# Optimization experiments

Hardware: AMD Instinct MI355X
Metric: run time of the kernel (lower is better)

## Reference

```python
import jax, jax.numpy as jnp
import numpy as np

EMBED_DIM = 1024
NUM_HEADS = 16
N_POS = 2048
BATCH = 4


def setup_inputs() -> dict:
    key = jax.random.key(0)
    k_x, k_w1, k_b1, k_wo, k_bo = jax.random.split(key, 5)
    s1 = 1.0 / np.sqrt(EMBED_DIM)
    x = jax.random.normal(k_x, (BATCH, N_POS, EMBED_DIM), dtype=jnp.float32)
    # torch Linear weights stored as [in, out] for x @ W + b
    W_qkv = jax.random.uniform(k_w1, (EMBED_DIM, 3 * EMBED_DIM), dtype=jnp.float32, minval=-s1, maxval=s1)
    b_qkv = jax.random.uniform(k_b1, (3 * EMBED_DIM,), dtype=jnp.float32, minval=-s1, maxval=s1)
    W_o = jax.random.uniform(k_wo, (EMBED_DIM, EMBED_DIM), dtype=jnp.float32, minval=-s1, maxval=s1)
    b_o = jax.random.uniform(k_bo, (EMBED_DIM,), dtype=jnp.float32, minval=-s1, maxval=s1)
    return {"x": x, "W_qkv": W_qkv, "b_qkv": b_qkv, "W_o": W_o, "b_o": b_o}


def reference(x, W_qkv, b_qkv, W_o, b_o):
    B, N, C = x.shape
    H = NUM_HEADS
    d_k = C // H
    qkv = x @ W_qkv + b_qkv                       # [B, N, 3C]
    q, k, v = jnp.split(qkv, 3, axis=-1)
    q = q.reshape(B, N, H, d_k).transpose(0, 2, 1, 3)  # [B, H, N, d_k]
    k = k.reshape(B, N, H, d_k).transpose(0, 2, 1, 3)
    v = v.reshape(B, N, H, d_k).transpose(0, 2, 1, 3)
    scores = jnp.einsum('bhqd,bhkd->bhqk', q, k) * (1.0 / np.sqrt(d_k))
    causal = jnp.tril(jnp.ones((N, N), dtype=bool))
    scores = jnp.where(causal, scores, -jnp.inf)
    attn = jax.nn.softmax(scores, axis=-1)
    out = jnp.einsum('bhqk,bhkd->bhqd', attn, v)  # [B, H, N, d_k]
    out = out.transpose(0, 2, 1, 3).reshape(B, N, C)
    return out @ W_o + b_o
```

## Files before the change

kernel.cpp:

```cpp
#include <hip/hip_runtime.h>
#include <hip/hip_bf16.h>

typedef __attribute__((ext_vector_type(8))) __bf16 bf16x8;
typedef __attribute__((ext_vector_type(4))) float f32x4;
typedef __attribute__((ext_vector_type(16))) float f32x16;
typedef __attribute__((ext_vector_type(4))) unsigned short u16x4;
typedef __attribute__((ext_vector_type(8))) unsigned short u16x8;
typedef __attribute__((ext_vector_type(4))) unsigned int u32x4;
typedef unsigned short u16;

#define MFMA16 __builtin_amdgcn_mfma_f32_16x16x32_bf16
#define MFMA32 __builtin_amdgcn_mfma_f32_32x32x16_bf16

#if __has_builtin(__builtin_amdgcn_exp2f)
#define EXP2F __builtin_amdgcn_exp2f
#else
#define EXP2F(x) __expf((x) * 0.69314718056f)
#endif

__device__ inline u16 f32_to_bf16_bits(float f) {
    unsigned u = __builtin_bit_cast(unsigned, f);
    unsigned r = u + 0x7FFFu + ((u >> 16) & 1u);
    return (u16)(r >> 16);
}

__device__ inline void g2l16(const void* g, void* l) {
    __builtin_amdgcn_global_load_lds(
        (const __attribute__((address_space(1))) unsigned int*)g,
        (__attribute__((address_space(3))) unsigned int*)l,
        16, 0, 0);
}

__device__ inline float red32_max(float x) { return fmaxf(x, __shfl_xor(x, 32)); }
__device__ inline float red32_sum(float x) { return x + __shfl_xor(x, 32); }

__global__ void cvt_bf16_kernel(const float* __restrict__ in, u16* __restrict__ out, int n) {
    int i = (blockIdx.x * 256 + threadIdx.x) * 8;
    if (i >= n) return;
    f32x4 v0 = *(const f32x4*)&in[i];
    f32x4 v1 = *(const f32x4*)&in[i + 4];
    u16x8 r;
#pragma unroll
    for (int j = 0; j < 4; ++j) {
        r[j] = f32_to_bf16_bits(v0[j]);
        r[j + 4] = f32_to_bf16_bits(v1[j]);
    }
    *(u16x8*)&out[i] = r;
}

__global__ __launch_bounds__(256) void cvt_t2_kernel(
    const float* __restrict__ W1, u16* __restrict__ WT1, int N1,
    const float* __restrict__ W2, u16* __restrict__ WT2, int N2, int K)
{
    int bx = blockIdx.x;
    const float* W; u16* WT; int N;
    const int nb1 = N1 >> 6;
    if (bx < nb1) { W = W1; WT = WT1; N = N1; }
    else          { W = W2; WT = WT2; N = N2; bx -= nb1; }
    const int w = threadIdx.x >> 6, l = threadIdx.x & 63;
    const int n = bx * 64 + l;
    const int k0 = blockIdx.y * 32 + w * 8;
    u16x8 r;
#pragma unroll
    for (int i = 0; i < 8; ++i)
        r[i] = f32_to_bf16_bits(W[(size_t)(k0 + i) * N + n]);
    *(u16x8*)&WT[(size_t)n * K + k0] = r;
}

template <int STORE_BF16>
__global__ __launch_bounds__(512) void gemm_8p2(
    const u16* __restrict__ A, const u16* __restrict__ BT,
    const float* __restrict__ bias, void* __restrict__ Cv,
    int M, int N, int K, int qcols, float qscale)
{
    __shared__ __align__(16) u16 SM[49152];
    const int tid = threadIdx.x;
    const int w = tid >> 6, l = tid & 63;
    const int lr = l & 15, lh = l >> 4;
    const int wr = (w >> 2) * 64;
    const int wc = (w & 3) * 64;

    const int xcd = blockIdx.x & 7;
    const int jb = blockIdx.x >> 3;
    const int g = jb >> 4;
    const int r = jb & 15;
    const int m0 = (xcd * 8 + (r >> 1)) * 128;
    const int n0 = (g * 2 + (r & 1)) * 256;

    const int NT = K >> 6;

    const int f0 = tid, f1 = 512 + tid;
    const int r0 = f0 >> 3, r1 = f1 >> 3;
    const int c0 = ((f0 & 7) ^ (r0 & 7)) * 8;

#define STAGE_CHUNK(j, c)                                                       \
    do {                                                                        \
        const int kk_ = (j) * 64;                                               \
        u16* db_ = SM + (((j) & 1) * 24576) + (c) * 8192;                       \
        const u16* base_ = ((c) == 0) ? (A + (size_t)m0 * K)                    \
                                      : (BT + (size_t)(n0 + ((c)-1) * 128) * K);\
        g2l16(base_ + (size_t)r0 * K + kk_ + c0, db_ + f0 * 8);                 \
        g2l16(base_ + (size_t)r1 * K + kk_ + c0, db_ + f1 * 8);                 \
    } while (0)

    f32x4 acc[4][4];
#pragma unroll
    for (int m = 0; m < 4; ++m)
#pragma unroll
        for (int n = 0; n < 4; ++n) acc[m][n] = (f32x4)(0.0f);

    STAGE_CHUNK(0, 0); STAGE_CHUNK(0, 1); STAGE_CHUNK(0, 2);

    const int swk = lr & 7;
    for (int j = 0; j < NT; ++j) {
        const u16* Ab = SM + (j & 1) * 24576;
        const u16* Bb = Ab + 8192;

        if (j + 1 < NT) {
            STAGE_CHUNK(j + 1, 0);
            asm volatile("s_waitcnt vmcnt(2)\n\ts_barrier" ::: "memory");
        } else {
            asm volatile("s_waitcnt vmcnt(0)\n\ts_barrier" ::: "memory");
        }

        bf16x8 af[4][2], bfr[2][2];
#pragma unroll
        for (int m = 0; m < 4; ++m) {
            const int row = wr + m * 16 + lr;
#pragma unroll
            for (int ks = 0; ks < 2; ++ks)
                af[m][ks] = *(const bf16x8*)&Ab[row * 64 + (((ks * 4 + lh) ^ swk) << 3)];
        }
#pragma unroll
        for (int n = 0; n < 2; ++n) {
            const int row = wc + n * 16 + lr;
#pragma unroll
            for (int ks = 0; ks < 2; ++ks)
                bfr[n][ks] = *(const bf16x8*)&Bb[row * 64 + (((ks * 4 + lh) ^ swk) << 3)];
        }
        if (j + 1 < NT) STAGE_CHUNK(j + 1, 1);

        asm volatile("s_barrier\n\ts_waitcnt lgkmcnt(0)" ::: "memory");
        __builtin_amdgcn_s_setprio(1);
#pragma unroll
        for (int m = 0; m < 4; ++m)
#pragma unroll
            for (int n = 0; n < 2; ++n)
#pragma unroll
                for (int ks = 0; ks < 2; ++ks)
                    acc[m][n] = MFMA16(af[m][ks], bfr[n][ks], acc[m][n], 0, 0, 0);
        __builtin_amdgcn_s_setprio(0);
        asm volatile("s_barrier" ::: "memory");

#pragma unroll
        for (int n = 0; n < 2; ++n) {
            const int row = wc + (n + 2) * 16 + lr;
#pragma unroll
            for (int ks = 0; ks < 2; ++ks)
                bfr[n][ks] = *(const bf16x8*)&Bb[row * 64 + (((ks * 4 + lh) ^ swk) << 3)];
        }
        if (j + 1 < NT) STAGE_CHUNK(j + 1, 2);

        asm volatile("s_barrier\n\ts_waitcnt lgkmcnt(0)" ::: "memory");
        __builtin_amdgcn_s_setprio(1);
#pragma unroll
        for (int m = 0; m < 4; ++m)
#pragma unroll
            for (int n = 0; n < 2; ++n)
#pragma unroll
                for (int ks = 0; ks < 2; ++ks)
                    acc[m][n + 2] = MFMA16(af[m][ks], bfr[n][ks], acc[m][n + 2], 0, 0, 0);
        __builtin_amdgcn_s_setprio(0);
        asm volatile("s_barrier" ::: "memory");
    }
#undef STAGE_CHUNK

#pragma unroll
    for (int m = 0; m < 4; ++m) {
        int row = m0 + wr + m * 16 + lh * 4;
#pragma unroll
        for (int n = 0; n < 4; ++n) {
            int col = n0 + wc + n * 16 + lr;
            float bs = bias[col];
            float sc = (col < qcols) ? qscale : 1.0f;
#pragma unroll
            for (int j2 = 0; j2 < 4; ++j2) {
                float v = (acc[m][n][j2] + bs) * sc;
                if (STORE_BF16)
                    ((u16*)Cv)[(size_t)(row + j2) * N + col] = f32_to_bf16_bits(v);
                else
                    ((float*)Cv)[(size_t)(row + j2) * N + col] = v;
            }
        }
    }
}

template <int STORE_BF16>
__global__ __launch_bounds__(256) void gemm_nt(
    const u16* __restrict__ A, const u16* __restrict__ BT,
    const float* __restrict__ bias, void* __restrict__ Cv,
    int M, int N, int K, int qcols, float qscale, int nbx)
{
    __shared__ __align__(16) u16 SM[24576];
    const int tid = threadIdx.x;
    const int w = tid >> 6, l = tid & 63;
    const int lr = l & 15, lh = l >> 4;
    const int wr = (w >> 1) * 64, wc = (w & 1) * 64;

    const int xcd = blockIdx.x & 7;
    const int j = blockIdx.x >> 3;
    const int g = j >> 5;
    const int r = j & 31;
    const int m0 = (xcd * 8 + (r >> 2)) * 128;
    const int n0 = (g * 4 + (r & 3)) * 128;
    (void)nbx;

    const int NT = K >> 5;

    const int f0 = tid, f1 = 256 + tid;
    const int r0 = f0 >> 2, r1 = f1 >> 2;
    const int cs0 = ((f0 & 3) ^ ((r0 >> 1) & 3)) * 8;
    const int cs1 = ((f1 & 3) ^ ((r1 >> 1) & 3)) * 8;
    const size_t arow0 = (size_t)(m0 + r0) * K, arow1 = (size_t)(m0 + r1) * K;
    const size_t brow0 = (size_t)(n0 + r0) * K, brow1 = (size_t)(n0 + r1) * K;

#define STAGE_TILE(t, set)                                                     \
    do {                                                                       \
        const int kk_ = (t) * 32;                                              \
        u16* dst_ = SM + (set) * 8192 + w * 512;                               \
        g2l16(A + arow0 + kk_ + cs0, dst_);                                    \
        g2l16(BT + brow0 + kk_ + cs0, dst_ + 4096);                            \
        g2l16(A + arow1 + kk_ + cs1, dst_ + 2048);                             \
        g2l16(BT + brow1 + kk_ + cs1, dst_ + 4096 + 2048);                     \
    } while (0)

    f32x4 acc[4][4];
#pragma unroll
    for (int m = 0; m < 4; ++m)
#pragma unroll
        for (int n = 0; n < 4; ++n) acc[m][n] = (f32x4)(0.0f);

    STAGE_TILE(0, 0);
    STAGE_TILE(1, 1);
    asm volatile("s_waitcnt vmcnt(4) lgkmcnt(0)\n\ts_barrier" ::: "memory");

    const int csw = (lr >> 1) & 3;
    int s0 = 0, s2 = 2;
    for (int t = 0; t < NT; ++t) {
        if (t + 2 < NT) STAGE_TILE(t + 2, s2);

        const u16* As = SM + s0 * 8192;
        const u16* Bs = As + 4096;
        bf16x8 af[4], bfr[4];
#pragma unroll
        for (int m = 0; m < 4; ++m)
            af[m] = *(const bf16x8*)&As[(wr + m * 16 + lr) * 32 + ((lh ^ csw) << 3)];
#pragma unroll
        for (int n = 0; n < 4; ++n)
            bfr[n] = *(const bf16x8*)&Bs[(wc + n * 16 + lr) * 32 + ((lh ^ csw) << 3)];
        __builtin_amdgcn_s_setprio(1);
#pragma unroll
        for (int m = 0; m < 4; ++m)
#pragma unroll
            for (int n = 0; n < 4; ++n)
                acc[m][n] = MFMA16(af[m], bfr[n], acc[m][n], 0, 0, 0);
        __builtin_amdgcn_s_setprio(0);

        if (t + 2 < NT)
            asm volatile("s_waitcnt vmcnt(4) lgkmcnt(0)\n\ts_barrier" ::: "memory");
        else if (t + 1 < NT)
            asm volatile("s_waitcnt vmcnt(0) lgkmcnt(0)\n\ts_barrier" ::: "memory");

        s0 = (s0 == 2) ? 0 : s0 + 1;
        s2 = (s2 == 2) ? 0 : s2 + 1;
    }
#undef STAGE_TILE

#pragma unroll
    for (int m = 0; m < 4; ++m) {
        int row = m0 + wr + m * 16 + lh * 4;
#pragma unroll
        for (int n = 0; n < 4; ++n) {
            int col = n0 + wc + n * 16 + lr;
            float bs = bias[col];
            float sc = (col < qcols) ? qscale : 1.0f;
#pragma unroll
            for (int j2 = 0; j2 < 4; ++j2) {
                float v = (acc[m][n][j2] + bs) * sc;
                if (STORE_BF16)
                    ((u16*)Cv)[(size_t)(row + j2) * N + col] = f32_to_bf16_bits(v);
                else
                    ((float*)Cv)[(size_t)(row + j2) * N + col] = v;
            }
        }
    }
}

__global__ __launch_bounds__(512, 1) void attn_kernel(
    const u16* __restrict__ qkv, u16* __restrict__ ctx)
{
    __shared__ __align__(16) u16 SM[32768];

    const int bid = blockIdx.x;
    const int xcd = bid & 7, jj = bid >> 3;
    const int bh = xcd * 8 + (jj >> 2);
    const int pr = jj & 3;
    const int b = bh >> 4, h = bh & 15;
    const size_t rowbase = (size_t)b * 2048;
    const int tid = threadIdx.x, w = tid >> 6, l = tid & 63;
    const int lq = l & 31, lk = l >> 5;

    const int rsub = l >> 3;
    const int cstage = l & 7;
    const int kchunk = cstage ^ rsub;

    bf16x8 vreg[2];

#pragma unroll
    for (int pass = 0; pass < 2; ++pass) {
        const int qt = pass ? (7 - pr) : pr;
        const int q0 = qt * 256;
        const int nt = 2 * qt + 2;
        const int qbase = q0 + w * 32;

        const u16* qp = qkv + (rowbase + qbase + lq) * 3072 + h * 64 + lk * 8;
        bf16x8 qf[4];
#pragma unroll
        for (int j = 0; j < 4; ++j) qf[j] = *(const bf16x8*)(qp + j * 16);

        f32x16 ot[2];
#pragma unroll
        for (int dt = 0; dt < 2; ++dt) ot[dt] = (f32x16)(0.0f);
        float m_run = -3e38f, l_run = 0.0f;

        __syncthreads();
#pragma unroll
        for (int p = 0; p < 2; ++p) {
            const int r = w * 16 + p * 8 + rsub;
            g2l16(qkv + (rowbase + r) * 3072 + 1024 + h * 64 + kchunk * 8,
                  SM + w * 1024 + p * 512);
            vreg[p] = *(const bf16x8*)(qkv + (rowbase + r) * 3072 + 2048 + h * 64 + cstage * 8);
        }
        asm volatile("s_waitcnt vmcnt(0)" ::: "memory");
#pragma unroll
        for (int p = 0; p < 2; ++p) {
            const int r = w * 16 + p * 8 + rsub;
#pragma unroll
            for (int i = 0; i < 8; ++i) {
                const int d = cstage * 8 + i;
                SM[16384 + ((d * 128 + r) ^ (((i ^ cstage) & 7) << 3))] = ((const u16*)&vreg[p])[i];
            }
        }
        __syncthreads();

        for (int t = 0; t < nt; ++t) {
            const int c = t & 1;
            const int kb = t * 128;
            u16* const Kb = SM + (c ? 8192 : 0);
            u16* const Vb = SM + 16384 + (c ? 8192 : 0);

            if (t + 1 < nt) {
                const int kb2 = kb + 128;
#pragma unroll
                for (int p = 0; p < 2; ++p) {
                    const int r = w * 16 + p * 8 + rsub;
                    g2l16(qkv + (rowbase + kb2 + r) * 3072 + 1024 + h * 64 + kchunk * 8,
                          SM + (c ? 0 : 8192) + w * 1024 + p * 512);
                    vreg[p] = *(const bf16x8*)(qkv + (rowbase + kb2 + r) * 3072 + 2048 + h * 64 + cstage * 8);
                }
            }

            if (kb <= qbase + 31) {
                bf16x8 kf[4][4];
#pragma unroll
                for (int kt = 0; kt < 4; ++kt)
#pragma unroll
                    for (int j = 0; j < 4; ++j)
                        kf[kt][j] = *(const bf16x8*)&Kb[((kt * 32 + lq) * 64 + j * 16 + lk * 8) ^ ((lq & 7) << 3)];

                f32x16 sf[4];
                __builtin_amdgcn_s_setprio(1);
#pragma unroll
                for (int kt = 0; kt < 4; ++kt) {
                    f32x16 z = (f32x16)(0.0f);
#pragma unroll
                    for (int j = 0; j < 4; ++j) z = MFMA32(kf[kt][j], qf[j], z, 0, 0, 0);
                    sf[kt] = z;
                }
                __builtin_amdgcn_s_setprio(0);

                float mt = -3e38f;
                if (kb + 127 > qbase) {
                    const int qrow = qbase + lq;
#pragma unroll
                    for (int kt = 0; kt < 4; ++kt)
#pragma unroll
                        for (int r = 0; r < 16; ++r) {
                            const int key = kb + kt * 32 + (r & 3) + 8 * (r >> 2) + 4 * lk;
                            float v = sf[kt][r];
                            if (key > qrow) v = -3e38f;
                            sf[kt][r] = v;
                            mt = fmaxf(mt, v);
                        }
                } else {
#pragma unroll
                    for (int kt = 0; kt < 4; ++kt)
#pragma unroll
                        for (int r = 0; r < 16; ++r) mt = fmaxf(mt, sf[kt][r]);
                }
                mt = red32_max(mt);

                const bool defer = __all(mt <= m_run + 16.0f);
                float mn = m_run;
                if (!defer) {
                    mn = fmaxf(m_run, mt);
                    const float alpha = EXP2F(m_run - mn);
                    m_run = mn;
                    l_run *= alpha;
#pragma unroll
                    for (int dt = 0; dt < 2; ++dt)
#pragma unroll
                        for (int r = 0; r < 16; ++r) ot[dt][r] *= alpha;
                }
                float rs = 0.0f;
#pragma unroll
                for (int kt = 0; kt < 4; ++kt)
#pragma unroll
                    for (int r = 0; r < 16; ++r) {
                        const float pp = EXP2F(sf[kt][r] - mn);
                        sf[kt][r] = pp;
                        rs += pp;
                    }
                l_run += red32_sum(rs);

                unsigned pc[4][4][2];
#pragma unroll
                for (int kt = 0; kt < 4; ++kt)
#pragma unroll
                    for (int rg = 0; rg < 4; ++rg) {
                        unsigned d0, d1;
                        asm("v_cvt_pk_bf16_f32 %0, %1, %2"
                            : "=v"(d0) : "v"((float)sf[kt][rg * 4 + 0]), "v"((float)sf[kt][rg * 4 + 1]));
                        asm("v_cvt_pk_bf16_f32 %0, %1, %2"
                            : "=v"(d1) : "v"((float)sf[kt][rg * 4 + 2]), "v"((float)sf[kt][rg * 4 + 3]));
                        pc[kt][rg][0] = d0;
                        pc[kt][rg][1] = d1;
                    }

                __builtin_amdgcn_s_setprio(1);
#pragma unroll
                for (int kt = 0; kt < 4; ++kt)
#pragma unroll
                    for (int hh = 0; hh < 2; ++hh) {
                        unsigned a0 = pc[kt][2 * hh][0], a1 = pc[kt][2 * hh][1];
                        unsigned b0 = pc[kt][2 * hh + 1][0], b1 = pc[kt][2 * hh + 1][1];
                        asm("v_permlane32_swap_b32 %0, %1" : "+v"(a0), "+v"(b0));
                        asm("v_permlane32_swap_b32 %0, %1" : "+v"(a1), "+v"(b1));
                        u32x4 wv = {a0, a1, b0, b1};
                        const bf16x8 pb = __builtin_bit_cast(bf16x8, wv);
                        const int k0 = 2 * kt + hh;
#pragma unroll
                        for (int dt = 0; dt < 2; ++dt) {
                            const int d = dt * 32 + lq;
                            const int vswz = ((d & 7) ^ (d >> 3)) & 7;
                            const bf16x8 vf = *(const bf16x8*)&Vb[((d * 128) + (k0 * 16 + lk * 8)) ^ (vswz << 3)];
                            ot[dt] = MFMA32(vf, pb, ot[dt], 0, 0, 0);
                        }
                    }
                __builtin_amdgcn_s_setprio(0);
            }

            asm volatile("s_waitcnt vmcnt(0)" ::: "memory");
            if (t + 1 < nt) {
                u16* const Vn = SM + 16384 + (c ? 0 : 8192);
#pragma unroll
                for (int p = 0; p < 2; ++p) {
                    const int r = w * 16 + p * 8 + rsub;
#pragma unroll
                    for (int i = 0; i < 8; ++i) {
                        const int d = cstage * 8 + i;
                        Vn[((d * 128 + r) ^ (((i ^ cstage) & 7) << 3))] = ((const u16*)&vreg[p])[i];
                    }
                }
            }
            __syncthreads();
        }

        u16* const out_l = SM + w * 2176;
        const float inv = 1.0f / l_run;
#pragma unroll
        for (int dt = 0; dt < 2; ++dt)
#pragma unroll
            for (int r = 0; r < 16; ++r) {
                const int d = dt * 32 + (r & 3) + 8 * (r >> 2) + 4 * lk;
                out_l[lq * 68 + d] = f32_to_bf16_bits(ot[dt][r] * inv);
            }
#pragma unroll
        for (int rr = 0; rr < 4; ++rr) {
            const int row = rr * 8 + (l >> 3);
            const bf16x8 v = *(const bf16x8*)&out_l[row * 68 + (l & 7) * 8];
            *(bf16x8*)(ctx + (rowbase + qbase + row) * 1024 + h * 64 + (l & 7) * 8) = v;
        }
    }
}

extern "C" void kernel_launch(void* const* d_in, const int* in_sizes, int n_in,
                              void* d_out, int out_size, void* d_ws, size_t ws_size,
                              hipStream_t stream) {
    const float* x      = (const float*)d_in[0];
    const float* W_qkv  = (const float*)d_in[1];
    const float* b_qkv  = (const float*)d_in[2];
    const float* W_o    = (const float*)d_in[3];
    const float* b_o    = (const float*)d_in[4];
    float* out = (float*)d_out;

    const int M = 4 * 2048;
    const int C = 1024;
    u16* qkv   = (u16*)d_ws;
    u16* xb    = qkv   + (size_t)M * 3 * C;
    u16* wqkvt = xb    + (size_t)M * C;
    u16* ctx   = wqkvt + (size_t)3 * C * C;
    u16* wot   = ctx   + (size_t)M * C;

    const float SCQ = 0.125f * 1.44269504089f;

    cvt_bf16_kernel<<<(M * C) / (256 * 8), 256, 0, stream>>>(x, xb, M * C);
    cvt_t2_kernel<<<dim3(3 * C / 64 + C / 64, C / 32), 256, 0, stream>>>(
        W_qkv, wqkvt, 3 * C, W_o, wot, C, C);

    gemm_8p2<1><<<(M / 128) * (3 * C / 256), 512, 0, stream>>>(xb, wqkvt, b_qkv, qkv,
                                                               M, 3 * C, C, C, SCQ);

    attn_kernel<<<256, 512, 0, stream>>>(qkv, ctx);

    gemm_nt<0><<<(C / 128) * (M / 128), 256, 0, stream>>>(ctx, wot, b_o, out,
                                                          M, C, C, 0, 1.0f, C / 128);
}
```

Measured before the change: 160.7 us.

## Split attention passes into separate blocks and reuse 8-phase GEMM for output projection

The attention kernel no longer loops over two causal query tiles per block. It launches 512 blocks, each handling one tile, with launch bounds allowing two blocks per CU, which aims for more occupancy and better overlap between blocks. The output projection now uses the existing gemm_8p2 kernel with 256-wide tiles instead of the separate gemm_nt kernel, and gemm_nt is removed. The risk is register pressure under the 2-block bound, and losing the paired light/heavy tile balance inside each block.

```diff
diff --git a/kernel.cpp b/kernel.cpp
--- a/kernel.cpp
+++ b/kernel.cpp
@@ -195,116 +195,18 @@
     }
 }
 
-template <int STORE_BF16>
-__global__ __launch_bounds__(256) void gemm_nt(
-    const u16* __restrict__ A, const u16* __restrict__ BT,
-    const float* __restrict__ bias, void* __restrict__ Cv,
-    int M, int N, int K, int qcols, float qscale, int nbx)
-{
-    __shared__ __align__(16) u16 SM[24576];
-    const int tid = threadIdx.x;
-    const int w = tid >> 6, l = tid & 63;
-    const int lr = l & 15, lh = l >> 4;
-    const int wr = (w >> 1) * 64, wc = (w & 1) * 64;
-
-    const int xcd = blockIdx.x & 7;
-    const int j = blockIdx.x >> 3;
-    const int g = j >> 5;
-    const int r = j & 31;
-    const int m0 = (xcd * 8 + (r >> 2)) * 128;
-    const int n0 = (g * 4 + (r & 3)) * 128;
-    (void)nbx;
-
-    const int NT = K >> 5;
-
-    const int f0 = tid, f1 = 256 + tid;
-    const int r0 = f0 >> 2, r1 = f1 >> 2;
-    const int cs0 = ((f0 & 3) ^ ((r0 >> 1) & 3)) * 8;
-    const int cs1 = ((f1 & 3) ^ ((r1 >> 1) & 3)) * 8;
-    const size_t arow0 = (size_t)(m0 + r0) * K, arow1 = (size_t)(m0 + r1) * K;
-    const size_t brow0 = (size_t)(n0 + r0) * K, brow1 = (size_t)(n0 + r1) * K;
-
-#define STAGE_TILE(t, set)                                                     \
-    do {                                                                       \
-        const int kk_ = (t) * 32;                                              \
-        u16* dst_ = SM + (set) * 8192 + w * 512;                               \
-        g2l16(A + arow0 + kk_ + cs0, dst_);                                    \
-        g2l16(BT + brow0 + kk_ + cs0, dst_ + 4096);                            \
-        g2l16(A + arow1 + kk_ + cs1, dst_ + 2048);                             \
-        g2l16(BT + brow1 + kk_ + cs1, dst_ + 4096 + 2048);                     \
-    } while (0)
-
-    f32x4 acc[4][4];
-#pragma unroll
-    for (int m = 0; m < 4; ++m)
-#pragma unroll
-        for (int n = 0; n < 4; ++n) acc[m][n] = (f32x4)(0.0f);
-
-    STAGE_TILE(0, 0);
-    STAGE_TILE(1, 1);
-    asm volatile("s_waitcnt vmcnt(4) lgkmcnt(0)\n\ts_barrier" ::: "memory");
-
-    const int csw = (lr >> 1) & 3;
-    int s0 = 0, s2 = 2;
-    for (int t = 0; t < NT; ++t) {
-        if (t + 2 < NT) STAGE_TILE(t + 2, s2);
-
-        const u16* As = SM + s0 * 8192;
-        const u16* Bs = As + 4096;
-        bf16x8 af[4], bfr[4];
-#pragma unroll
-        for (int m = 0; m < 4; ++m)
-            af[m] = *(const bf16x8*)&As[(wr + m * 16 + lr) * 32 + ((lh ^ csw) << 3)];
-#pragma unroll
-        for (int n = 0; n < 4; ++n)
-            bfr[n] = *(const bf16x8*)&Bs[(wc + n * 16 + lr) * 32 + ((lh ^ csw) << 3)];
-        __builtin_amdgcn_s_setprio(1);
-#pragma unroll
-        for (int m = 0; m < 4; ++m)
-#pragma unroll
-            for (int n = 0; n < 4; ++n)
-                acc[m][n] = MFMA16(af[m], bfr[n], acc[m][n], 0, 0, 0);
-        __builtin_amdgcn_s_setprio(0);
-
-        if (t + 2 < NT)
-            asm volatile("s_waitcnt vmcnt(4) lgkmcnt(0)\n\ts_barrier" ::: "memory");
-        else if (t + 1 < NT)
-            asm volatile("s_waitcnt vmcnt(0) lgkmcnt(0)\n\ts_barrier" ::: "memory");
-
-        s0 = (s0 == 2) ? 0 : s0 + 1;
-        s2 = (s2 == 2) ? 0 : s2 + 1;
-    }
-#undef STAGE_TILE
-
-#pragma unroll
-    for (int m = 0; m < 4; ++m) {
-        int row = m0 + wr + m * 16 + lh * 4;
-#pragma unroll
-        for (int n = 0; n < 4; ++n) {
-            int col = n0 + wc + n * 16 + lr;
-            float bs = bias[col];
-            float sc = (col < qcols) ? qscale : 1.0f;
-#pragma unroll
-            for (int j2 = 0; j2 < 4; ++j2) {
-                float v = (acc[m][n][j2] + bs) * sc;
-                if (STORE_BF16)
-                    ((u16*)Cv)[(size_t)(row + j2) * N + col] = f32_to_bf16_bits(v);
-                else
-                    ((float*)Cv)[(size_t)(row + j2) * N + col] = v;
-            }
-        }
-    }
-}
-
-__global__ __launch_bounds__(512, 1) void attn_kernel(
+__global__ __launch_bounds__(512, 2) void attn_kernel(
     const u16* __restrict__ qkv, u16* __restrict__ ctx)
 {
     __shared__ __align__(16) u16 SM[32768];
 
     const int bid = blockIdx.x;
-    const int xcd = bid & 7, jj = bid >> 3;
+    const int half = bid >> 8;
+    const int base = bid & 255;
+    const int xcd = base & 7, jj = base >> 3;
     const int bh = xcd * 8 + (jj >> 2);
     const int pr = jj & 3;
+    const int qt = half ? (7 - pr) : pr;
     const int b = bh >> 4, h = bh & 15;
     const size_t rowbase = (size_t)b * 2048;
     const int tid = threadIdx.x, w = tid >> 6, l = tid & 63;
@@ -316,191 +218,186 @@
 
     bf16x8 vreg[2];
 
-#pragma unroll
-    for (int pass = 0; pass < 2; ++pass) {
-        const int qt = pass ? (7 - pr) : pr;
-        const int q0 = qt * 256;
-        const int nt = 2 * qt + 2;
-        const int qbase = q0 + w * 32;
-
-        const u16* qp = qkv + (rowbase + qbase + lq) * 3072 + h * 64 + lk * 8;
-        bf16x8 qf[4];
-#pragma unroll
-        for (int j = 0; j < 4; ++j) qf[j] = *(const bf16x8*)(qp + j * 16);
-
-        f32x16 ot[2];
-#pragma unroll
-        for (int dt = 0; dt < 2; ++dt) ot[dt] = (f32x16)(0.0f);
-        float m_run = -3e38f, l_run = 0.0f;
-
-        __syncthreads();
-#pragma unroll
-        for (int p = 0; p < 2; ++p) {
-            const int r = w * 16 + p * 8 + rsub;
-            g2l16(qkv + (rowbase + r) * 3072 + 1024 + h * 64 + kchunk * 8,
-                  SM + w * 1024 + p * 512);
-            vreg[p] = *(const bf16x8*)(qkv + (rowbase + r) * 3072 + 2048 + h * 64 + cstage * 8);
-        }
-        asm volatile("s_waitcnt vmcnt(0)" ::: "memory");
-#pragma unroll
-        for (int p = 0; p < 2; ++p) {
-            const int r = w * 16 + p * 8 + rsub;
-#pragma unroll
-            for (int i = 0; i < 8; ++i) {
-                const int d = cstage * 8 + i;
-                SM[16384 + ((d * 128 + r) ^ (((i ^ cstage) & 7) << 3))] = ((const u16*)&vreg[p])[i];
-            }
-        }
-        __syncthreads();
-
-        for (int t = 0; t < nt; ++t) {
-            const int c = t & 1;
-            const int kb = t * 128;
-            u16* const Kb = SM + (c ? 8192 : 0);
-            u16* const Vb = SM + 16384 + (c ? 8192 : 0);
-
-            if (t + 1 < nt) {
-                const int kb2 = kb + 128;
-#pragma unroll
-                for (int p = 0; p < 2; ++p) {
-                    const int r = w * 16 + p * 8 + rsub;
-                    g2l16(qkv + (rowbase + kb2 + r) * 3072 + 1024 + h * 64 + kchunk * 8,
-                          SM + (c ? 0 : 8192) + w * 1024 + p * 512);
-                    vreg[p] = *(const bf16x8*)(qkv + (rowbase + kb2 + r) * 3072 + 2048 + h * 64 + cstage * 8);
+    const int q0 = qt * 256;
+    const int nt = 2 * qt + 2;
+    const int qbase = q0 + w * 32;
+
+    const u16* qp = qkv + (rowbase + qbase + lq) * 3072 + h * 64 + lk * 8;
+    bf16x8 qf[4];
+#pragma unroll
+    for (int j = 0; j < 4; ++j) qf[j] = *(const bf16x8*)(qp + j * 16);
+
+    f32x16 ot[2];
+#pragma unroll
+    for (int dt = 0; dt < 2; ++dt) ot[dt] = (f32x16)(0.0f);
+    float m_run = -3e38f, l_run = 0.0f;
+
+#pragma unroll
+    for (int p = 0; p < 2; ++p) {
+        const int r = w * 16 + p * 8 + rsub;
+        g2l16(qkv + (rowbase + r) * 3072 + 1024 + h * 64 + kchunk * 8,
+              SM + w * 1024 + p * 512);
+        vreg[p] = *(const bf16x8*)(qkv + (rowbase + r) * 3072 + 2048 + h * 64 + cstage * 8);
+    }
+    asm volatile("s_waitcnt vmcnt(0)" ::: "memory");
+#pragma unroll
+    for (int p = 0; p < 2; ++p) {
+        const int r = w * 16 + p * 8 + rsub;
+#pragma unroll
+        for (int i = 0; i < 8; ++i) {
+            const int d = cstage * 8 + i;
+            SM[16384 + ((d * 128 + r) ^ (((i ^ cstage) & 7) << 3))] = ((const u16*)&vreg[p])[i];
+        }
+    }
+    __syncthreads();
+
+    for (int t = 0; t < nt; ++t) {
+        const int c = t & 1;
+        const int kb = t * 128;
+        u16* const Kb = SM + (c ? 8192 : 0);
+        u16* const Vb = SM + 16384 + (c ? 8192 : 0);
+
+        if (t + 1 < nt) {
+            const int kb2 = kb + 128;
+#pragma unroll
+            for (int p = 0; p < 2; ++p) {
+                const int r = w * 16 + p * 8 + rsub;
+                g2l16(qkv + (rowbase + kb2 + r) * 3072 + 1024 + h * 64 + kchunk * 8,
+                      SM + (c ? 0 : 8192) + w * 1024 + p * 512);
+                vreg[p] = *(const bf16x8*)(qkv + (rowbase + kb2 + r) * 3072 + 2048 + h * 64 + cstage * 8);
+            }
+        }
+
+        if (kb <= qbase + 31) {
+            bf16x8 kf[4][4];
+#pragma unroll
+            for (int kt = 0; kt < 4; ++kt)
+#pragma unroll
+                for (int j = 0; j < 4; ++j)
+                    kf[kt][j] = *(const bf16x8*)&Kb[((kt * 32 + lq) * 64 + j * 16 + lk * 8) ^ ((lq & 7) << 3)];
+
+            f32x16 sf[4];
+            __builtin_amdgcn_s_setprio(1);
+#pragma unroll
+            for (int kt = 0; kt < 4; ++kt) {
+                f32x16 z = (f32x16)(0.0f);
+#pragma unroll
+                for (int j = 0; j < 4; ++j) z = MFMA32(kf[kt][j], qf[j], z, 0, 0, 0);
+                sf[kt] = z;
+            }
+            __builtin_amdgcn_s_setprio(0);
+
+            float mt = -3e38f;
+            if (kb + 127 > qbase) {
+                const int qrow = qbase + lq;
+#pragma unroll
+                for (int kt = 0; kt < 4; ++kt)
+#pragma unroll
+                    for (int r = 0; r < 16; ++r) {
+                        const int key = kb + kt * 32 + (r & 3) + 8 * (r >> 2) + 4 * lk;
+                        float v = sf[kt][r];
+                        if (key > qrow) v = -3e38f;
+                        sf[kt][r] = v;
+                        mt = fmaxf(mt, v);
+                    }
+            } else {
+#pragma unroll
+                for (int kt = 0; kt < 4; ++kt)
+#pragma unroll
+                    for (int r = 0; r < 16; ++r) mt = fmaxf(mt, sf[kt][r]);
+            }
+            mt = red32_max(mt);
+
+            const bool defer = __all(mt <= m_run + 16.0f);
+            float mn = m_run;
+            if (!defer) {
+                mn = fmaxf(m_run, mt);
+                const float alpha = EXP2F(m_run - mn);
+                m_run = mn;
+                l_run *= alpha;
+#pragma unroll
+                for (int dt = 0; dt < 2; ++dt)
+#pragma unroll
+                    for (int r = 0; r < 16; ++r) ot[dt][r] *= alpha;
+            }
+            float rs = 0.0f;
+#pragma unroll
+            for (int kt = 0; kt < 4; ++kt)
+#pragma unroll
+                for (int r = 0; r < 16; ++r) {
+                    const float pp = EXP2F(sf[kt][r] - mn);
+                    sf[kt][r] = pp;
+                    rs += pp;
                 }
-            }
-
-            if (kb <= qbase + 31) {
-                bf16x8 kf[4][4];
-#pragma unroll
-                for (int kt = 0; kt < 4; ++kt)
-#pragma unroll
-                    for (int j = 0; j < 4; ++j)
-                        kf[kt][j] = *(const bf16x8*)&Kb[((kt * 32 + lq) * 64 + j * 16 + lk * 8) ^ ((lq & 7) << 3)];
-
-                f32x16 sf[4];
-                __builtin_amdgcn_s_setprio(1);
-#pragma unroll
-                for (int kt = 0; kt < 4; ++kt) {
-                    f32x16 z = (f32x16)(0.0f);
-#pragma unroll
-                    for (int j = 0; j < 4; ++j) z = MFMA32(kf[kt][j], qf[j], z, 0, 0, 0);
-                    sf[kt] = z;
+            l_run += red32_sum(rs);
+
+            unsigned pc[4][4][2];
+#pragma unroll
+            for (int kt = 0; kt < 4; ++kt)
+#pragma unroll
+                for (int rg = 0; rg < 4; ++rg) {
+                    unsigned d0, d1;
+                    asm("v_cvt_pk_bf16_f32 %0, %1, %2"
+                        : "=v"(d0) : "v"((float)sf[kt][rg * 4 + 0]), "v"((float)sf[kt][rg * 4 + 1]));
+                    asm("v_cvt_pk_bf16_f32 %0, %1, %2"
+                        : "=v"(d1) : "v"((float)sf[kt][rg * 4 + 2]), "v"((float)sf[kt][rg * 4 + 3]));
+                    pc[kt][rg][0] = d0;
+                    pc[kt][rg][1] = d1;
                 }
-                __builtin_amdgcn_s_setprio(0);
-
-                float mt = -3e38f;
-                if (kb + 127 > qbase) {
-                    const int qrow = qbase + lq;
-#pragma unroll
-                    for (int kt = 0; kt < 4; ++kt)
-#pragma unroll
-                        for (int r = 0; r < 16; ++r) {
-                            const int key = kb + kt * 32 + (r & 3) + 8 * (r >> 2) + 4 * lk;
-                            float v = sf[kt][r];
-                            if (key > qrow) v = -3e38f;
-                            sf[kt][r] = v;
-                            mt = fmaxf(mt, v);
-                        }
-                } else {
-#pragma unroll
-                    for (int kt = 0; kt < 4; ++kt)
-#pragma unroll
-                        for (int r = 0; r < 16; ++r) mt = fmaxf(mt, sf[kt][r]);
-                }
-                mt = red32_max(mt);
-
-                const bool defer = __all(mt <= m_run + 16.0f);
-                float mn = m_run;
-                if (!defer) {
-                    mn = fmaxf(m_run, mt);
-                    const float alpha = EXP2F(m_run - mn);
-                    m_run = mn;
-                    l_run *= alpha;
-#pragma unroll
-                    for (int dt = 0; dt < 2; ++dt)
-#pragma unroll
-                        for (int r = 0; r < 16; ++r) ot[dt][r] *= alpha;
-                }
-                float rs = 0.0f;
-#pragma unroll
-                for (int kt = 0; kt < 4; ++kt)
-#pragma unroll
-                    for (int r = 0; r < 16; ++r) {
-                        const float pp = EXP2F(sf[kt][r] - mn);
-                        sf[kt][r] = pp;
-                        rs += pp;
-                    }
-                l_run += red32_sum(rs);
-
-                unsigned pc[4][4][2];
-#pragma unroll
-                for (int kt = 0; kt < 4; ++kt)
-#pragma unroll
-                    for (int rg = 0; rg < 4; ++rg) {
-                        unsigned d0, d1;
-                        asm("v_cvt_pk_bf16_f32 %0, %1, %2"
-                            : "=v"(d0) : "v"((float)sf[kt][rg * 4 + 0]), "v"((float)sf[kt][rg * 4 + 1]));
-                        asm("v_cvt_pk_bf16_f32 %0, %1, %2"
-                            : "=v"(d1) : "v"((float)sf[kt][rg * 4 + 2]), "v"((float)sf[kt][rg * 4 + 3]));
-                        pc[kt][rg][0] = d0;
-                        pc[kt][rg][1] = d1;
-                    }
-
-                __builtin_amdgcn_s_setprio(1);
-#pragma unroll
-                for (int kt = 0; kt < 4; ++kt)
-#pragma unroll
-                    for (int hh = 0; hh < 2; ++hh) {
-                        unsigned a0 = pc[kt][2 * hh][0], a1 = pc[kt][2 * hh][1];
-                        unsigned b0 = pc[kt][2 * hh + 1][0], b1 = pc[kt][2 * hh + 1][1];
-                        asm("v_permlane32_swap_b32 %0, %1" : "+v"(a0), "+v"(b0));
-                        asm("v_permlane32_swap_b32 %0, %1" : "+v"(a1), "+v"(b1));
-                        u32x4 wv = {a0, a1, b0, b1};
-                        const bf16x8 pb = __builtin_bit_cast(bf16x8, wv);
-                        const int k0 = 2 * kt + hh;
-#pragma unroll
-                        for (int dt = 0; dt < 2; ++dt) {
-                            const int d = dt * 32 + lq;
-                            const int vswz = ((d & 7) ^ (d >> 3)) & 7;
-                            const bf16x8 vf = *(const bf16x8*)&Vb[((d * 128) + (k0 * 16 + lk * 8)) ^ (vswz << 3)];
-                            ot[dt] = MFMA32(vf, pb, ot[dt], 0, 0, 0);
-                        }
-                    }
-                __builtin_amdgcn_s_setprio(0);
-            }
-
-            asm volatile("s_waitcnt vmcnt(0)" ::: "memory");
-            if (t + 1 < nt) {
-                u16* const Vn = SM + 16384 + (c ? 0 : 8192);
-#pragma unroll
-                for (int p = 0; p < 2; ++p) {
-                    const int r = w * 16 + p * 8 + rsub;
-#pragma unroll
-                    for (int i = 0; i < 8; ++i) {
-                        const int d = cstage * 8 + i;
-                        Vn[((d * 128 + r) ^ (((i ^ cstage) & 7) << 3))] = ((const u16*)&vreg[p])[i];
+
+            __builtin_amdgcn_s_setprio(1);
+#pragma unroll
+            for (int kt = 0; kt < 4; ++kt)
+#pragma unroll
+                for (int hh = 0; hh < 2; ++hh) {
+                    unsigned a0 = pc[kt][2 * hh][0], a1 = pc[kt][2 * hh][1];
+                    unsigned b0 = pc[kt][2 * hh + 1][0], b1 = pc[kt][2 * hh + 1][1];
+                    asm("v_permlane32_swap_b32 %0, %1" : "+v"(a0), "+v"(b0));
+                    asm("v_permlane32_swap_b32 %0, %1" : "+v"(a1), "+v"(b1));
+                    u32x4 wv = {a0, a1, b0, b1};
+                    const bf16x8 pb = __builtin_bit_cast(bf16x8, wv);
+                    const int k0 = 2 * kt + hh;
+#pragma unroll
+                    for (int dt = 0; dt < 2; ++dt) {
+                        const int d = dt * 32 + lq;
+                        const int vswz = ((d & 7) ^ (d >> 3)) & 7;
+                        const bf16x8 vf = *(const bf16x8*)&Vb[((d * 128) + (k0 * 16 + lk * 8)) ^ (vswz << 3)];
+                        ot[dt] = MFMA32(vf, pb, ot[dt], 0, 0, 0);
                     }
                 }
-            }
-            __syncthreads();
-        }
-
-        u16* const out_l = SM + w * 2176;
-        const float inv = 1.0f / l_run;
-#pragma unroll
-        for (int dt = 0; dt < 2; ++dt)
-#pragma unroll
-            for (int r = 0; r < 16; ++r) {
-                const int d = dt * 32 + (r & 3) + 8 * (r >> 2) + 4 * lk;
-                out_l[lq * 68 + d] = f32_to_bf16_bits(ot[dt][r] * inv);
-            }
-#pragma unroll
-        for (int rr = 0; rr < 4; ++rr) {
-            const int row = rr * 8 + (l >> 3);
-            const bf16x8 v = *(const bf16x8*)&out_l[row * 68 + (l & 7) * 8];
-            *(bf16x8*)(ctx + (rowbase + qbase + row) * 1024 + h * 64 + (l & 7) * 8) = v;
-        }
+            __builtin_amdgcn_s_setprio(0);
+        }
+
+        asm volatile("s_waitcnt vmcnt(0)" ::: "memory");
+        if (t + 1 < nt) {
+            u16* const Vn = SM + 16384 + (c ? 0 : 8192);
+#pragma unroll
+            for (int p = 0; p < 2; ++p) {
+                const int r = w * 16 + p * 8 + rsub;
+#pragma unroll
+                for (int i = 0; i < 8; ++i) {
+                    const int d = cstage * 8 + i;
+                    Vn[((d * 128 + r) ^ (((i ^ cstage) & 7) << 3))] = ((const u16*)&vreg[p])[i];
+                }
+            }
+        }
+        __syncthreads();
+    }
+
+    u16* const out_l = SM + w * 2176;
+    const float inv = 1.0f / l_run;
+#pragma unroll
+    for (int dt = 0; dt < 2; ++dt)
+#pragma unroll
+        for (int r = 0; r < 16; ++r) {
+            const int d = dt * 32 + (r & 3) + 8 * (r >> 2) + 4 * lk;
+            out_l[lq * 68 + d] = f32_to_bf16_bits(ot[dt][r] * inv);
+        }
+#pragma unroll
+    for (int rr = 0; rr < 4; ++rr) {
+        const int row = rr * 8 + (l >> 3);
+        const bf16x8 v = *(const bf16x8*)&out_l[row * 68 + (l & 7) * 8];
+        *(bf16x8*)(ctx + (rowbase + qbase + row) * 1024 + h * 64 + (l & 7) * 8) = v;
     }
 }
 
@@ -531,8 +428,8 @@
     gemm_8p2<1><<<(M / 128) * (3 * C / 256), 512, 0, stream>>>(xb, wqkvt, b_qkv, qkv,
                                                                M, 3 * C, C, C, SCQ);
 
-    attn_kernel<<<256, 512, 0, stream>>>(qkv, ctx);
-
-    gemm_nt<0><<<(C / 128) * (M / 128), 256, 0, stream>>>(ctx, wot, b_o, out,
-                                                          M, C, C, 0, 1.0f, C / 128);
-}
+    attn_kernel<<<512, 512, 0, stream>>>(qkv, ctx);
+
+    gemm_8p2<0><<<(M / 128) * (C / 256), 512, 0, stream>>>(ctx, wot, b_o, out,
+                                                           M, C, C, 0, 1.0f);
+}
```

Measured after the change: 175.4 us. 9.2% more time.
